# Kernel optimization log

Hardware: AMD Instinct MI355X
Metric: run time of the kernel (lower is better)

Reference implementation:

```python
import jax, jax.numpy as jnp
import numpy as np

N_NODES = 10000
N_EDGES = 70000
H = 128
L = 15  # message_passing_num
NODE_IN = 11  # 2 frame dims + 9 one-hot node types
EDGE_IN = 3
LN_EPS = 1e-5


def _mlp(x, W1, b1, W2, b2):
    return jax.nn.relu(x @ W1 + b1) @ W2 + b2


def _mlp_ln(x, W1, b1, W2, b2, g, b):
    h = _mlp(x, W1, b1, W2, b2)
    mu = jnp.mean(h, axis=-1, keepdims=True)
    var = jnp.var(h, axis=-1, keepdims=True)
    return (h - mu) * jax.lax.rsqrt(var + LN_EPS) * g + b


def setup_inputs() -> dict:
    key = jax.random.key(0)
    ks = iter(jax.random.split(key, 40))
    rn = lambda shp, s: (jax.random.normal(next(ks), shp, jnp.float32) * s)
    inp = {
        "node_type": jax.random.randint(next(ks), (N_NODES,), 0, 9, jnp.int32),
        "edge_index": jax.random.randint(next(ks), (2, N_EDGES), 0, N_NODES, jnp.int32),
        "frames": jax.random.normal(next(ks), (N_NODES, 2), jnp.float32),
        "edge_feats": jax.random.normal(next(ks), (N_EDGES, EDGE_IN), jnp.float32),
        "node_norm_mean": jax.random.normal(next(ks), (NODE_IN,), jnp.float32) * 0.1,
        "node_norm_std": jax.random.uniform(next(ks), (NODE_IN,), jnp.float32) + 0.5,
        "out_norm_mean": jax.random.normal(next(ks), (2,), jnp.float32) * 0.1,
        "out_norm_std": jax.random.uniform(next(ks), (2,), jnp.float32) + 0.5,
        # encoder node MLP (11 -> 128 -> 128, LayerNorm)
        "enc_nW1": rn((NODE_IN, H), NODE_IN ** -0.5), "enc_nb1": jnp.zeros((H,)),
        "enc_nW2": rn((H, H), H ** -0.5), "enc_nb2": jnp.zeros((H,)),
        "enc_nlng": jnp.ones((H,)), "enc_nlnb": jnp.zeros((H,)),
        # encoder edge MLP (3 -> 128 -> 128, LayerNorm)
        "enc_eW1": rn((EDGE_IN, H), EDGE_IN ** -0.5), "enc_eb1": jnp.zeros((H,)),
        "enc_eW2": rn((H, H), H ** -0.5), "enc_eb2": jnp.zeros((H,)),
        "enc_elng": jnp.ones((H,)), "enc_elnb": jnp.zeros((H,)),
        # L GNN blocks, stacked. Edge MLP: 3H -> H -> H (+LN); Node MLP: 2H -> H -> H (+LN)
        "eb_W1": rn((L, 3 * H, H), (3 * H) ** -0.5), "eb_b1": jnp.zeros((L, H)),
        "eb_W2": rn((L, H, H), H ** -0.5), "eb_b2": jnp.zeros((L, H)),
        "eb_lng": jnp.ones((L, H)), "eb_lnb": jnp.zeros((L, H)),
        "nb_W1": rn((L, 2 * H, H), (2 * H) ** -0.5), "nb_b1": jnp.zeros((L, H)),
        "nb_W2": rn((L, H, H), H ** -0.5), "nb_b2": jnp.zeros((L, H)),
        "nb_lng": jnp.ones((L, H)), "nb_lnb": jnp.zeros((L, H)),
        # decoder MLP (128 -> 128 -> 2, no LayerNorm)
        "dec_W1": rn((H, H), H ** -0.5), "dec_b1": jnp.zeros((H,)),
        "dec_W2": rn((H, 2), H ** -0.5), "dec_b2": jnp.zeros((2,)),
    }
    return inp


def reference(node_type, edge_index, frames, edge_feats,
              node_norm_mean, node_norm_std, out_norm_mean, out_norm_std,
              enc_nW1, enc_nb1, enc_nW2, enc_nb2, enc_nlng, enc_nlnb,
              enc_eW1, enc_eb1, enc_eW2, enc_eb2, enc_elng, enc_elnb,
              eb_W1, eb_b1, eb_W2, eb_b2, eb_lng, eb_lnb,
              nb_W1, nb_b1, nb_W2, nb_b2, nb_lng, nb_lnb,
              dec_W1, dec_b1, dec_W2, dec_b2):
    n_nodes = frames.shape[0]
    senders, receivers = edge_index[0], edge_index[1]

    # update_node_attr: concat(frames, one_hot(type, 9)) then normalize (eval mode)
    one_hot = jax.nn.one_hot(node_type, 9, dtype=frames.dtype)
    node_feats = jnp.concatenate([frames, one_hot], axis=1)  # [N, 11]
    node_attr = (node_feats - node_norm_mean) / node_norm_std

    # Encoder
    x = _mlp_ln(node_attr, enc_nW1, enc_nb1, enc_nW2, enc_nb2, enc_nlng, enc_nlnb)   # [N, H]
    e = _mlp_ln(edge_feats, enc_eW1, enc_eb1, enc_eW2, enc_eb2, enc_elng, enc_elnb)  # [E, H]

    # Processor: L residual GNN blocks (EdgeBlock then NodeBlock)
    def block(carry, p):
        x, e = carry
        (eW1, eb1, eW2, eb2, eg, ebn, nW1, nb1, nW2, nb2, ng, nbn) = p
        e_in = jnp.concatenate([x[senders], x[receivers], e], axis=-1)  # [E, 3H]
        e_new = _mlp_ln(e_in, eW1, eb1, eW2, eb2, eg, ebn)              # [E, H]
        agg = jax.ops.segment_sum(e_new, receivers, num_segments=n_nodes)  # [N, H]
        x_new = _mlp_ln(jnp.concatenate([x, agg], axis=-1), nW1, nb1, nW2, nb2, ng, nbn)
        return (x + x_new, e + e_new), None

    (x, e), _ = jax.lax.scan(
        block, (x, e),
        (eb_W1, eb_b1, eb_W2, eb_b2, eb_lng, eb_lnb,
         nb_W1, nb_b1, nb_W2, nb_b2, nb_lng, nb_lnb))

    # Decoder (no LayerNorm) + inverse output normalization (eval path)
    decoded = _mlp(x, dec_W1, dec_b1, dec_W2, dec_b2)  # [N, 2]
    velocity_update = decoded * out_norm_std + out_norm_mean
    return frames + velocity_update
```

## Files before the change

kernel.cpp:

```cpp
#include <hip/hip_runtime.h>
#include <hip/hip_bf16.h>

#define N_NODES 10000
#define N_EDGES 70000
#define NPAD 10112
#define EPAD 70016
#define H 128
#define NLAYERS 15
constexpr float LN_EPS = 1e-5f;

typedef __attribute__((ext_vector_type(8))) short short8;
typedef __attribute__((ext_vector_type(4))) float f32x4;

__device__ __forceinline__ float bf2f(unsigned int ulo16) {
    return __uint_as_float(ulo16 << 16);
}
__device__ __forceinline__ unsigned short f2bf(float f) {
    unsigned int x = __float_as_uint(f);
    x += 0x7fffu + ((x >> 16) & 1u);
    return (unsigned short)(x >> 16);
}

__global__ void prep_node(const int* __restrict__ nt, const float* __restrict__ frames,
                          const float* __restrict__ nm, const float* __restrict__ ns,
                          unsigned short* __restrict__ a16b) {
    int i = blockIdx.x * blockDim.x + threadIdx.x;
    if (i >= NPAD * 32) return;
    int n = i >> 5, k = i & 31;
    float v = 0.f;
    if (n < N_NODES && k < 11) {
        float raw = (k < 2) ? frames[n * 2 + k] : ((nt[n] == (k - 2)) ? 1.f : 0.f);
        v = (raw - nm[k]) / ns[k];
    }
    a16b[i] = f2bf(v);
}

__global__ void prep_edge(const float* __restrict__ ef, unsigned short* __restrict__ a4b) {
    int i = blockIdx.x * blockDim.x + threadIdx.x;
    if (i >= EPAD * 32) return;
    int e = i >> 5, k = i & 31;
    float v = (e < N_EDGES && k < 3) ? ef[e * 3 + k] : 0.f;
    a4b[i] = f2bf(v);
}

__global__ void transpose_w(const float* __restrict__ w, unsigned short* __restrict__ wt,
                            int Kr, int Kp, int nmat) {
    int i = blockIdx.x * blockDim.x + threadIdx.x;
    int total = nmat * 128 * Kp;
    if (i >= total) return;
    int m = i / (128 * Kp);
    int r = i % (128 * Kp);
    int c = r / Kp;
    int k = r % Kp;
    float v = (k < Kr) ? w[((size_t)m * Kr + k) * H + c] : 0.f;
    wt[i] = f2bf(v);
}

__global__ void hist_kernel(const int* __restrict__ rcv, int* __restrict__ counts) {
    int j = blockIdx.x * blockDim.x + threadIdx.x;
    if (j < N_EDGES) atomicAdd(&counts[rcv[j]], 1);
}

__global__ void scan_kernel(const int* __restrict__ counts, int* __restrict__ starts) {
    __shared__ int part[1024];
    const int CH = 10;
    int t = threadIdx.x;
    int base = t * CH;
    int loc[CH];
    int s = 0;
#pragma unroll
    for (int i = 0; i < CH; i++) {
        int idx = base + i;
        int c = (idx < N_NODES) ? counts[idx] : 0;
        loc[i] = s;
        s += c;
    }
    part[t] = s;
    __syncthreads();
    for (int off = 1; off < 1024; off <<= 1) {
        int v = (t >= off) ? part[t - off] : 0;
        __syncthreads();
        part[t] += v;
        __syncthreads();
    }
    int pre = (t > 0) ? part[t - 1] : 0;
#pragma unroll
    for (int i = 0; i < CH; i++) {
        int idx = base + i;
        if (idx < N_NODES) starts[idx] = pre + loc[i];
    }
}

__global__ void scatter_kernel(const int* __restrict__ rcv, const int* __restrict__ starts,
                               int* __restrict__ cursor, int* __restrict__ esorted) {
    int j = blockIdx.x * blockDim.x + threadIdx.x;
    if (j >= N_EDGES) return;
    int r = rcv[j];
    int p = starts[r] + atomicAdd(&cursor[r], 1);
    esorted[p] = j;
}

__global__ void agg_kernel(const unsigned short* __restrict__ enew,
                           const int* __restrict__ esorted,
                           const int* __restrict__ starts,
                           const int* __restrict__ counts,
                           unsigned short* __restrict__ aggb) {
    int n = blockIdx.x * 8 + (threadIdx.x >> 5);
    int l = threadIdx.x & 31;
    if (n >= N_NODES) return;
    float a0 = 0.f, a1 = 0.f, a2 = 0.f, a3 = 0.f;
    int s0 = starts[n], cnt = counts[n];
    for (int j = 0; j < cnt; ++j) {
        int e = esorted[s0 + j];
        uint2 v = *reinterpret_cast<const uint2*>(enew + (size_t)e * H + l * 4);
        a0 += bf2f(v.x & 0xffffu);
        a1 += bf2f(v.x >> 16);
        a2 += bf2f(v.y & 0xffffu);
        a3 += bf2f(v.y >> 16);
    }
    uint2 o;
    o.x = (unsigned int)f2bf(a0) | ((unsigned int)f2bf(a1) << 16);
    o.y = (unsigned int)f2bf(a2) | ((unsigned int)f2bf(a3) << 16);
    *reinterpret_cast<uint2*>(aggb + (size_t)n * H + l * 4) = o;
}

template <int K, int AMODE, int EPI, int WR>
__launch_bounds__(256)
__global__ void gemm_mfma(const unsigned short* __restrict__ A,
                          const unsigned short* __restrict__ Xb,
                          const unsigned short* __restrict__ Eb,
                          const unsigned short* __restrict__ Gb,
                          const int* __restrict__ snd,
                          const int* __restrict__ rcv,
                          const unsigned short* __restrict__ Bt,
                          const float* __restrict__ bias,
                          const float* __restrict__ lng,
                          const float* __restrict__ lnb,
                          unsigned short* __restrict__ out_bf,
                          float* __restrict__ out_fp,
                          unsigned short* __restrict__ enew_bf,
                          int nrows) {
    constexpr int BK = (K >= 64) ? 64 : K;
    constexpr int SA = BK + 8;
    constexpr int BM = 64 * WR;
    constexpr int KSTEP = BK / 32;
    __shared__ __attribute__((aligned(16))) unsigned short As[BM * SA];
    __shared__ __attribute__((aligned(16))) unsigned short Bs[H * SA];

    const int tid = threadIdx.x;
    const int wave = tid >> 6;
    const int lane = tid & 63;
    const int l15 = lane & 15;
    const int lhi = lane >> 4;
    const int row0 = blockIdx.x * BM;
    const int wrow = wave * 16 * WR;

    f32x4 acc[WR][8];
#pragma unroll
    for (int i = 0; i < WR; i++)
#pragma unroll
        for (int j = 0; j < 8; j++) acc[i][j] = (f32x4){0.f, 0.f, 0.f, 0.f};

    for (int kc = 0; kc < K; kc += BK) {
        constexpr int KQ = BK / 8;
        constexpr int LPT_A = BM * BK / 8 / 256;
#pragma unroll
        for (int it = 0; it < LPT_A; ++it) {
            int q = tid + it * 256;
            int r = q / KQ;
            int kq = q % KQ;
            int gk = kc + kq * 8;
            int grow = row0 + r;
            const unsigned short* src;
            if (AMODE == 0) {
                src = A + (size_t)grow * K + gk;
            } else if (AMODE == 1) {
                int e = (grow < nrows) ? grow : 0;
                if (gk < H)          src = Xb + (size_t)snd[e] * H + gk;
                else if (gk < 2 * H) src = Xb + (size_t)rcv[e] * H + (gk - H);
                else                 src = Eb + (size_t)grow * H + (gk - 2 * H);
            } else {
                if (gk < H) src = Xb + (size_t)grow * H + gk;
                else        src = Gb + (size_t)grow * H + (gk - H);
            }
            uint4 v = *reinterpret_cast<const uint4*>(src);
            *reinterpret_cast<uint4*>(&As[r * SA + kq * 8]) = v;
        }
        constexpr int LPT_B = H * BK / 8 / 256;
#pragma unroll
        for (int it = 0; it < LPT_B; ++it) {
            int q = tid + it * 256;
            int c = q / KQ;
            int kq = q % KQ;
            uint4 v = *reinterpret_cast<const uint4*>(Bt + (size_t)c * K + kc + kq * 8);
            *reinterpret_cast<uint4*>(&Bs[c * SA + kq * 8]) = v;
        }
        __syncthreads();
#pragma unroll
        for (int ks = 0; ks < KSTEP; ++ks) {
            short8 af[WR];
#pragma unroll
            for (int i = 0; i < WR; ++i)
                af[i] = *reinterpret_cast<const short8*>(
                    &As[(wrow + i * 16 + l15) * SA + ks * 32 + lhi * 8]);
#pragma unroll
            for (int j = 0; j < 8; ++j) {
                short8 bfr = *reinterpret_cast<const short8*>(
                    &Bs[(j * 16 + l15) * SA + ks * 32 + lhi * 8]);
#pragma unroll
                for (int i = 0; i < WR; ++i)
                    acc[i][j] = __builtin_amdgcn_mfma_f32_16x16x32_bf16(af[i], bfr, acc[i][j], 0, 0, 0);
            }
        }
        __syncthreads();
    }

    float bv[8], gv[8], lv[8];
#pragma unroll
    for (int j = 0; j < 8; ++j) {
        bv[j] = bias[j * 16 + l15];
        if (EPI >= 1) { gv[j] = lng[j * 16 + l15]; lv[j] = lnb[j * 16 + l15]; }
    }

#pragma unroll
    for (int i = 0; i < WR; ++i) {
#pragma unroll
        for (int r = 0; r < 4; ++r) {
            int row = row0 + wrow + i * 16 + lhi * 4 + r;
            if (EPI == 0) {
                if (row < nrows) {
#pragma unroll
                    for (int j = 0; j < 8; ++j) {
                        float v = acc[i][j][r] + bv[j];
                        v = v > 0.f ? v : 0.f;
                        out_bf[(size_t)row * H + j * 16 + l15] = f2bf(v);
                    }
                }
            } else {
                float v[8];
                float s = 0.f, s2 = 0.f;
#pragma unroll
                for (int j = 0; j < 8; ++j) {
                    v[j] = acc[i][j][r] + bv[j];
                    s += v[j];
                    s2 += v[j] * v[j];
                }
#pragma unroll
                for (int m = 1; m < 16; m <<= 1) {
                    s += __shfl_xor(s, m);
                    s2 += __shfl_xor(s2, m);
                }
                float mean = s * (1.f / 128.f);
                float var = s2 * (1.f / 128.f) - mean * mean;
                float rstd = rsqrtf(var + LN_EPS);
                if (row < nrows) {
#pragma unroll
                    for (int j = 0; j < 8; ++j) {
                        float o = (v[j] - mean) * rstd * gv[j] + lv[j];
                        size_t off = (size_t)row * H + j * 16 + l15;
                        if (EPI == 1) {
                            out_fp[off] = o;
                            out_bf[off] = f2bf(o);
                        } else if (EPI == 2) {
                            float nx = out_fp[off] + o;
                            out_fp[off] = nx;
                            out_bf[off] = f2bf(nx);
                        } else {
                            float ne = out_fp[off] + o;
                            out_fp[off] = ne;
                            out_bf[off] = f2bf(ne);
                            enew_bf[off] = f2bf(o);
                        }
                    }
                }
            }
        }
    }
}

__global__ void decoder_kernel(const float* __restrict__ x,
                               const float* __restrict__ frames,
                               const float* __restrict__ W1, const float* __restrict__ b1,
                               const float* __restrict__ W2, const float* __restrict__ b2,
                               const float* __restrict__ omean, const float* __restrict__ ostd,
                               float* __restrict__ outp) {
    __shared__ float xr[H];
    __shared__ float hr[H];
    __shared__ float red[2][2];
    int n = blockIdx.x;
    int t = threadIdx.x;
    xr[t] = x[n * H + t];
    __syncthreads();
    float acc = 0.f;
#pragma unroll 8
    for (int k = 0; k < H; k++) acc += xr[k] * W1[k * H + t];
    hr[t] = fmaxf(acc + b1[t], 0.f);
    __syncthreads();
    float p0 = hr[t] * W2[t * 2 + 0];
    float p1 = hr[t] * W2[t * 2 + 1];
#pragma unroll
    for (int m = 1; m < 64; m <<= 1) {
        p0 += __shfl_xor(p0, m);
        p1 += __shfl_xor(p1, m);
    }
    if ((t & 63) == 0) { red[t >> 6][0] = p0; red[t >> 6][1] = p1; }
    __syncthreads();
    if (t < 2) {
        float d = red[0][t] + red[1][t] + b2[t];
        outp[n * 2 + t] = frames[n * 2 + t] + d * ostd[t] + omean[t];
    }
}

extern "C" void kernel_launch(void* const* d_in, const int* in_sizes, int n_in,
                              void* d_out, int out_size, void* d_ws, size_t ws_size,
                              hipStream_t stream) {
    (void)in_sizes; (void)n_in; (void)out_size; (void)ws_size;
    const int*   node_type  = (const int*)  d_in[0];
    const int*   edge_index = (const int*)  d_in[1];
    const float* frames     = (const float*)d_in[2];
    const float* edge_feats = (const float*)d_in[3];
    const float* nmean      = (const float*)d_in[4];
    const float* nstd       = (const float*)d_in[5];
    const float* omean      = (const float*)d_in[6];
    const float* ostd       = (const float*)d_in[7];
    const float* enc_nW1    = (const float*)d_in[8];
    const float* enc_nb1    = (const float*)d_in[9];
    const float* enc_nW2    = (const float*)d_in[10];
    const float* enc_nb2    = (const float*)d_in[11];
    const float* enc_nlng   = (const float*)d_in[12];
    const float* enc_nlnb   = (const float*)d_in[13];
    const float* enc_eW1    = (const float*)d_in[14];
    const float* enc_eb1    = (const float*)d_in[15];
    const float* enc_eW2    = (const float*)d_in[16];
    const float* enc_eb2    = (const float*)d_in[17];
    const float* enc_elng   = (const float*)d_in[18];
    const float* enc_elnb   = (const float*)d_in[19];
    const float* eb_W1      = (const float*)d_in[20];
    const float* eb_b1      = (const float*)d_in[21];
    const float* eb_W2      = (const float*)d_in[22];
    const float* eb_b2      = (const float*)d_in[23];
    const float* eb_g       = (const float*)d_in[24];
    const float* eb_bn      = (const float*)d_in[25];
    const float* nb_W1      = (const float*)d_in[26];
    const float* nb_b1      = (const float*)d_in[27];
    const float* nb_W2      = (const float*)d_in[28];
    const float* nb_b2      = (const float*)d_in[29];
    const float* nb_g       = (const float*)d_in[30];
    const float* nb_bn      = (const float*)d_in[31];
    const float* dec_W1     = (const float*)d_in[32];
    const float* dec_b1     = (const float*)d_in[33];
    const float* dec_W2     = (const float*)d_in[34];
    const float* dec_b2     = (const float*)d_in[35];

    const int* snd = edge_index;
    const int* rcv = edge_index + N_EDGES;

    char* p = (char*)d_ws;
    auto alloc = [&](size_t bytes) {
        void* r = (void*)p;
        p += (bytes + 255) & ~(size_t)255;
        return r;
    };
    float* x_fp  = (float*)alloc((size_t)NPAD * H * 4);
    float* e_fp  = (float*)alloc((size_t)EPAD * H * 4);
    unsigned short* x_bf   = (unsigned short*)alloc((size_t)NPAD * H * 2);
    unsigned short* e_bf   = (unsigned short*)alloc((size_t)EPAD * H * 2);
    unsigned short* enew   = (unsigned short*)alloc((size_t)EPAD * H * 2);
    unsigned short* h_bf   = (unsigned short*)alloc((size_t)EPAD * H * 2);
    unsigned short* agg_bf = (unsigned short*)alloc((size_t)NPAD * H * 2);
    unsigned short* a16b   = (unsigned short*)alloc((size_t)NPAD * 32 * 2);
    unsigned short* a4b    = (unsigned short*)alloc((size_t)EPAD * 32 * 2);
    unsigned short* wt_en1 = (unsigned short*)alloc((size_t)128 * 32 * 2);
    unsigned short* wt_ee1 = (unsigned short*)alloc((size_t)128 * 32 * 2);
    unsigned short* wt_en2 = (unsigned short*)alloc((size_t)128 * 128 * 2);
    unsigned short* wt_ee2 = (unsigned short*)alloc((size_t)128 * 128 * 2);
    unsigned short* wt_eb1 = (unsigned short*)alloc((size_t)NLAYERS * 128 * 384 * 2);
    unsigned short* wt_eb2 = (unsigned short*)alloc((size_t)NLAYERS * 128 * 128 * 2);
    unsigned short* wt_nb1 = (unsigned short*)alloc((size_t)NLAYERS * 128 * 256 * 2);
    unsigned short* wt_nb2 = (unsigned short*)alloc((size_t)NLAYERS * 128 * 128 * 2);
    int* counts  = (int*)alloc((size_t)N_NODES * 4);
    int* starts  = (int*)alloc((size_t)N_NODES * 4);
    int* cursor  = (int*)alloc((size_t)N_NODES * 4);
    int* esorted = (int*)alloc((size_t)N_EDGES * 4);

    prep_node<<<(NPAD * 32 + 255) / 256, 256, 0, stream>>>(node_type, frames, nmean, nstd, a16b);
    prep_edge<<<(EPAD * 32 + 255) / 256, 256, 0, stream>>>(edge_feats, a4b);
    auto tw = [&](const float* w, unsigned short* wt, int Kr, int Kp, int nmat) {
        int total = nmat * 128 * Kp;
        transpose_w<<<(total + 255) / 256, 256, 0, stream>>>(w, wt, Kr, Kp, nmat);
    };
    tw(enc_nW1, wt_en1, 11, 32, 1);
    tw(enc_eW1, wt_ee1, 3, 32, 1);
    tw(enc_nW2, wt_en2, 128, 128, 1);
    tw(enc_eW2, wt_ee2, 128, 128, 1);
    tw(eb_W1, wt_eb1, 384, 384, NLAYERS);
    tw(eb_W2, wt_eb2, 128, 128, NLAYERS);
    tw(nb_W1, wt_nb1, 256, 256, NLAYERS);
    tw(nb_W2, wt_nb2, 128, 128, NLAYERS);

    hipMemsetAsync(counts, 0, (size_t)N_NODES * 4, stream);
    hipMemsetAsync(cursor, 0, (size_t)N_NODES * 4, stream);
    hist_kernel<<<(N_EDGES + 255) / 256, 256, 0, stream>>>(rcv, counts);
    scan_kernel<<<1, 1024, 0, stream>>>(counts, starts);
    scatter_kernel<<<(N_EDGES + 255) / 256, 256, 0, stream>>>(rcv, starts, cursor, esorted);

    const int gE = EPAD / 128;
    const int gN = NPAD / 64;
    const unsigned short* nu_ = nullptr;
    const int* ni_ = nullptr;
    const float* nf_ = nullptr;
    unsigned short* nm_ = nullptr;
    float* nfm_ = nullptr;

    gemm_mfma<32, 0, 0, 1><<<gN, 256, 0, stream>>>(a16b, nu_, nu_, nu_, ni_, ni_,
        wt_en1, enc_nb1, nf_, nf_, h_bf, nfm_, nm_, N_NODES);
    gemm_mfma<128, 0, 1, 1><<<gN, 256, 0, stream>>>(h_bf, nu_, nu_, nu_, ni_, ni_,
        wt_en2, enc_nb2, enc_nlng, enc_nlnb, x_bf, x_fp, nm_, N_NODES);
    gemm_mfma<32, 0, 0, 2><<<gE, 256, 0, stream>>>(a4b, nu_, nu_, nu_, ni_, ni_,
        wt_ee1, enc_eb1, nf_, nf_, h_bf, nfm_, nm_, N_EDGES);
    gemm_mfma<128, 0, 1, 2><<<gE, 256, 0, stream>>>(h_bf, nu_, nu_, nu_, ni_, ni_,
        wt_ee2, enc_eb2, enc_elng, enc_elnb, e_bf, e_fp, nm_, N_EDGES);

    for (int l = 0; l < NLAYERS; ++l) {
        gemm_mfma<384, 1, 0, 2><<<gE, 256, 0, stream>>>(nu_, x_bf, e_bf, nu_, snd, rcv,
            wt_eb1 + (size_t)l * 128 * 384, eb_b1 + l * H, nf_, nf_,
            h_bf, nfm_, nm_, N_EDGES);
        gemm_mfma<128, 0, 3, 2><<<gE, 256, 0, stream>>>(h_bf, nu_, nu_, nu_, ni_, ni_,
            wt_eb2 + (size_t)l * 128 * 128, eb_b2 + l * H, eb_g + l * H, eb_bn + l * H,
            e_bf, e_fp, enew, N_EDGES);
        agg_kernel<<<(N_NODES + 7) / 8, 256, 0, stream>>>(enew, esorted, starts, counts, agg_bf);
        gemm_mfma<256, 2, 0, 1><<<gN, 256, 0, stream>>>(nu_, x_bf, nu_, agg_bf, ni_, ni_,
            wt_nb1 + (size_t)l * 128 * 256, nb_b1 + l * H, nf_, nf_,
            h_bf, nfm_, nm_, N_NODES);
        gemm_mfma<128, 0, 2, 1><<<gN, 256, 0, stream>>>(h_bf, nu_, nu_, nu_, ni_, ni_,
            wt_nb2 + (size_t)l * 128 * 128, nb_b2 + l * H, nb_g + l * H, nb_bn + l * H,
            x_bf, x_fp, nm_, N_NODES);
    }

    decoder_kernel<<<N_NODES, 128, 0, stream>>>(x_fp, frames, dec_W1, dec_b1, dec_W2, dec_b2,
                                                omean, ostd, (float*)d_out);
}
```

Before: 1.460 ms.

## Fuse both MLP GEMMs into one kernel keeping hidden activations in LDS

Merges the two GEMMs of each MLP (first layer with ReLU, second layer with LayerNorm epilogue) into one kernel. The ReLU'd hidden tile is kept in shared memory and used directly as the A operand of the second GEMM, so the hidden h_bf buffer no longer round-trips through global memory and the launch count per layer halves. It also replaces the naive weight transpose with a shared-memory tiled transpose. The cost is more LDS per block (a hidden tile of up to 128x136 bf16 added), which may lower occupancy.

```diff
diff --git a/kernel.cpp b/kernel.cpp
--- a/kernel.cpp
+++ b/kernel.cpp
@@ -43,17 +43,29 @@
     a4b[i] = f2bf(v);
 }
 
-__global__ void transpose_w(const float* __restrict__ w, unsigned short* __restrict__ wt,
-                            int Kr, int Kp, int nmat) {
-    int i = blockIdx.x * blockDim.x + threadIdx.x;
-    int total = nmat * 128 * Kp;
-    if (i >= total) return;
-    int m = i / (128 * Kp);
-    int r = i % (128 * Kp);
-    int c = r / Kp;
-    int k = r % Kp;
-    float v = (k < Kr) ? w[((size_t)m * Kr + k) * H + c] : 0.f;
-    wt[i] = f2bf(v);
+__global__ void transpose_w_tiled(const float* __restrict__ w, unsigned short* __restrict__ wt,
+                                  int Kr, int Kp, int nmat) {
+    __shared__ float T[32][33];
+    int nkt = Kp / 32;
+    int bid = blockIdx.x;
+    int m = bid / (nkt * 4);
+    int rest = bid % (nkt * 4);
+    int kt = rest / 4, ct = rest % 4;
+    int t = threadIdx.x;
+    int tc = t & 31, tr = t >> 5;
+#pragma unroll
+    for (int rr = 0; rr < 4; ++rr) {
+        int k = kt * 32 + tr + rr * 8;
+        int c = ct * 32 + tc;
+        T[tr + rr * 8][tc] = (k < Kr) ? w[((size_t)m * Kr + k) * H + c] : 0.f;
+    }
+    __syncthreads();
+#pragma unroll
+    for (int rr = 0; rr < 4; ++rr) {
+        int c = ct * 32 + tr + rr * 8;
+        int k = kt * 32 + tc;
+        wt[((size_t)m * H + c) * Kp + k] = f2bf(T[tc][tr + rr * 8]);
+    }
 }
 
 __global__ void hist_kernel(const int* __restrict__ rcv, int* __restrict__ counts) {
@@ -124,28 +136,32 @@
     *reinterpret_cast<uint2*>(aggb + (size_t)n * H + l * 4) = o;
 }
 
-template <int K, int AMODE, int EPI, int WR>
+template <int K1, int AMODE, int EPI, int WR>
 __launch_bounds__(256)
-__global__ void gemm_mfma(const unsigned short* __restrict__ A,
+__global__ void mlp_fused(const unsigned short* __restrict__ A,
                           const unsigned short* __restrict__ Xb,
                           const unsigned short* __restrict__ Eb,
                           const unsigned short* __restrict__ Gb,
                           const int* __restrict__ snd,
                           const int* __restrict__ rcv,
-                          const unsigned short* __restrict__ Bt,
-                          const float* __restrict__ bias,
+                          const unsigned short* __restrict__ Bt1,
+                          const float* __restrict__ bias1,
+                          const unsigned short* __restrict__ Bt2,
+                          const float* __restrict__ bias2,
                           const float* __restrict__ lng,
                           const float* __restrict__ lnb,
                           unsigned short* __restrict__ out_bf,
                           float* __restrict__ out_fp,
                           unsigned short* __restrict__ enew_bf,
                           int nrows) {
-    constexpr int BK = (K >= 64) ? 64 : K;
-    constexpr int SA = BK + 8;
+    constexpr int BK1 = (K1 >= 64) ? 64 : K1;
+    constexpr int SA = BK1 + 8;
+    constexpr int SB = 72;
+    constexpr int SH = H + 8;
     constexpr int BM = 64 * WR;
-    constexpr int KSTEP = BK / 32;
     __shared__ __attribute__((aligned(16))) unsigned short As[BM * SA];
-    __shared__ __attribute__((aligned(16))) unsigned short Bs[H * SA];
+    __shared__ __attribute__((aligned(16))) unsigned short Bs[H * SB];
+    __shared__ __attribute__((aligned(16))) unsigned short Hs[BM * SH];
 
     const int tid = threadIdx.x;
     const int wave = tid >> 6;
@@ -161,9 +177,9 @@
 #pragma unroll
         for (int j = 0; j < 8; j++) acc[i][j] = (f32x4){0.f, 0.f, 0.f, 0.f};
 
-    for (int kc = 0; kc < K; kc += BK) {
-        constexpr int KQ = BK / 8;
-        constexpr int LPT_A = BM * BK / 8 / 256;
+    for (int kc = 0; kc < K1; kc += BK1) {
+        constexpr int KQ = BK1 / 8;
+        constexpr int LPT_A = BM * KQ / 256;
 #pragma unroll
         for (int it = 0; it < LPT_A; ++it) {
             int q = tid + it * 256;
@@ -173,7 +189,7 @@
             int grow = row0 + r;
             const unsigned short* src;
             if (AMODE == 0) {
-                src = A + (size_t)grow * K + gk;
+                src = A + (size_t)grow * K1 + gk;
             } else if (AMODE == 1) {
                 int e = (grow < nrows) ? grow : 0;
                 if (gk < H)          src = Xb + (size_t)snd[e] * H + gk;
@@ -186,18 +202,18 @@
             uint4 v = *reinterpret_cast<const uint4*>(src);
             *reinterpret_cast<uint4*>(&As[r * SA + kq * 8]) = v;
         }
-        constexpr int LPT_B = H * BK / 8 / 256;
+        constexpr int LPT_B = H * KQ / 256;
 #pragma unroll
         for (int it = 0; it < LPT_B; ++it) {
             int q = tid + it * 256;
             int c = q / KQ;
             int kq = q % KQ;
-            uint4 v = *reinterpret_cast<const uint4*>(Bt + (size_t)c * K + kc + kq * 8);
-            *reinterpret_cast<uint4*>(&Bs[c * SA + kq * 8]) = v;
-        }
-        __syncthreads();
-#pragma unroll
-        for (int ks = 0; ks < KSTEP; ++ks) {
+            uint4 v = *reinterpret_cast<const uint4*>(Bt1 + (size_t)c * K1 + kc + kq * 8);
+            *reinterpret_cast<uint4*>(&Bs[c * SB + kq * 8]) = v;
+        }
+        __syncthreads();
+#pragma unroll
+        for (int ks = 0; ks < BK1 / 32; ++ks) {
             short8 af[WR];
 #pragma unroll
             for (int i = 0; i < WR; ++i)
@@ -206,7 +222,7 @@
 #pragma unroll
             for (int j = 0; j < 8; ++j) {
                 short8 bfr = *reinterpret_cast<const short8*>(
-                    &Bs[(j * 16 + l15) * SA + ks * 32 + lhi * 8]);
+                    &Bs[(j * 16 + l15) * SB + ks * 32 + lhi * 8]);
 #pragma unroll
                 for (int i = 0; i < WR; ++i)
                     acc[i][j] = __builtin_amdgcn_mfma_f32_16x16x32_bf16(af[i], bfr, acc[i][j], 0, 0, 0);
@@ -215,11 +231,63 @@
         __syncthreads();
     }
 
+    {
+        float b1v[8];
+#pragma unroll
+        for (int j = 0; j < 8; ++j) b1v[j] = bias1[j * 16 + l15];
+#pragma unroll
+        for (int i = 0; i < WR; ++i)
+#pragma unroll
+            for (int r = 0; r < 4; ++r) {
+                int rl = wrow + i * 16 + lhi * 4 + r;
+#pragma unroll
+                for (int j = 0; j < 8; ++j) {
+                    float v = acc[i][j][r] + b1v[j];
+                    Hs[rl * SH + j * 16 + l15] = f2bf(v > 0.f ? v : 0.f);
+                }
+            }
+    }
+
+#pragma unroll
+    for (int i = 0; i < WR; i++)
+#pragma unroll
+        for (int j = 0; j < 8; j++) acc[i][j] = (f32x4){0.f, 0.f, 0.f, 0.f};
+
+    for (int kc = 0; kc < H; kc += 64) {
+        __syncthreads();
+#pragma unroll
+        for (int it = 0; it < 4; ++it) {
+            int q = tid + it * 256;
+            int c = q >> 3;
+            int kq = q & 7;
+            uint4 v = *reinterpret_cast<const uint4*>(Bt2 + (size_t)c * H + kc + kq * 8);
+            *reinterpret_cast<uint4*>(&Bs[c * SB + kq * 8]) = v;
+        }
+        __syncthreads();
+#pragma unroll
+        for (int ks = 0; ks < 2; ++ks) {
+            short8 af[WR];
+#pragma unroll
+            for (int i = 0; i < WR; ++i)
+                af[i] = *reinterpret_cast<const short8*>(
+                    &Hs[(wrow + i * 16 + l15) * SH + kc + ks * 32 + lhi * 8]);
+#pragma unroll
+            for (int j = 0; j < 8; ++j) {
+                short8 bfr = *reinterpret_cast<const short8*>(
+                    &Bs[(j * 16 + l15) * SB + ks * 32 + lhi * 8]);
+#pragma unroll
+                for (int i = 0; i < WR; ++i)
+                    acc[i][j] = __builtin_amdgcn_mfma_f32_16x16x32_bf16(af[i], bfr, acc[i][j], 0, 0, 0);
+            }
+        }
+    }
+
     float bv[8], gv[8], lv[8];
 #pragma unroll
     for (int j = 0; j < 8; ++j) {
-        bv[j] = bias[j * 16 + l15];
-        if (EPI >= 1) { gv[j] = lng[j * 16 + l15]; lv[j] = lnb[j * 16 + l15]; }
+        bv[j] = bias2[j * 16 + l15];
+        gv[j] = lng[j * 16 + l15];
+        lv[j] = lnb[j * 16 + l15];
     }
 
 #pragma unroll
@@ -227,50 +295,39 @@
 #pragma unroll
         for (int r = 0; r < 4; ++r) {
             int row = row0 + wrow + i * 16 + lhi * 4 + r;
-            if (EPI == 0) {
-                if (row < nrows) {
-#pragma unroll
-                    for (int j = 0; j < 8; ++j) {
-                        float v = acc[i][j][r] + bv[j];
-                        v = v > 0.f ? v : 0.f;
-                        out_bf[(size_t)row * H + j * 16 + l15] = f2bf(v);
-                    }
-                }
-            } else {
-                float v[8];
-                float s = 0.f, s2 = 0.f;
+            float v[8];
+            float s = 0.f, s2 = 0.f;
+#pragma unroll
+            for (int j = 0; j < 8; ++j) {
+                v[j] = acc[i][j][r] + bv[j];
+                s += v[j];
+                s2 += v[j] * v[j];
+            }
+#pragma unroll
+            for (int m = 1; m < 16; m <<= 1) {
+                s += __shfl_xor(s, m);
+                s2 += __shfl_xor(s2, m);
+            }
+            float mean = s * (1.f / 128.f);
+            float var = s2 * (1.f / 128.f) - mean * mean;
+            float rstd = rsqrtf(var + LN_EPS);
+            if (row < nrows) {
 #pragma unroll
                 for (int j = 0; j < 8; ++j) {
-                    v[j] = acc[i][j][r] + bv[j];
-                    s += v[j];
-                    s2 += v[j] * v[j];
-                }
-#pragma unroll
-                for (int m = 1; m < 16; m <<= 1) {
-                    s += __shfl_xor(s, m);
-                    s2 += __shfl_xor(s2, m);
-                }
-                float mean = s * (1.f / 128.f);
-                float var = s2 * (1.f / 128.f) - mean * mean;
-                float rstd = rsqrtf(var + LN_EPS);
-                if (row < nrows) {
-#pragma unroll
-                    for (int j = 0; j < 8; ++j) {
-                        float o = (v[j] - mean) * rstd * gv[j] + lv[j];
-                        size_t off = (size_t)row * H + j * 16 + l15;
-                        if (EPI == 1) {
-                            out_fp[off] = o;
-                            out_bf[off] = f2bf(o);
-                        } else if (EPI == 2) {
-                            float nx = out_fp[off] + o;
-                            out_fp[off] = nx;
-                            out_bf[off] = f2bf(nx);
-                        } else {
-                            float ne = out_fp[off] + o;
-                            out_fp[off] = ne;
-                            out_bf[off] = f2bf(ne);
-                            enew_bf[off] = f2bf(o);
-                        }
+                    float o = (v[j] - mean) * rstd * gv[j] + lv[j];
+                    size_t off = (size_t)row * H + j * 16 + l15;
+                    if (EPI == 1) {
+                        out_fp[off] = o;
+                        out_bf[off] = f2bf(o);
+                    } else if (EPI == 2) {
+                        float nx = out_fp[off] + o;
+                        out_fp[off] = nx;
+                        out_bf[off] = f2bf(nx);
+                    } else {
+                        float ne = out_fp[off] + o;
+                        out_fp[off] = ne;
+                        out_bf[off] = f2bf(ne);
+                        enew_bf[off] = f2bf(o);
                     }
                 }
             }
@@ -366,7 +423,6 @@
     unsigned short* x_bf   = (unsigned short*)alloc((size_t)NPAD * H * 2);
     unsigned short* e_bf   = (unsigned short*)alloc((size_t)EPAD * H * 2);
     unsigned short* enew   = (unsigned short*)alloc((size_t)EPAD * H * 2);
-    unsigned short* h_bf   = (unsigned short*)alloc((size_t)EPAD * H * 2);
     unsigned short* agg_bf = (unsigned short*)alloc((size_t)NPAD * H * 2);
     unsigned short* a16b   = (unsigned short*)alloc((size_t)NPAD * 32 * 2);
     unsigned short* a4b    = (unsigned short*)alloc((size_t)EPAD * 32 * 2);
@@ -386,8 +442,8 @@
     prep_node<<<(NPAD * 32 + 255) / 256, 256, 0, stream>>>(node_type, frames, nmean, nstd, a16b);
     prep_edge<<<(EPAD * 32 + 255) / 256, 256, 0, stream>>>(edge_feats, a4b);
     auto tw = [&](const float* w, unsigned short* wt, int Kr, int Kp, int nmat) {
-        int total = nmat * 128 * Kp;
-        transpose_w<<<(total + 255) / 256, 256, 0, stream>>>(w, wt, Kr, Kp, nmat);
+        int blocks = nmat * (Kp / 32) * 4;
+        transpose_w_tiled<<<blocks, 256, 0, stream>>>(w, wt, Kr, Kp, nmat);
     };
     tw(enc_nW1, wt_en1, 11, 32, 1);
     tw(enc_eW1, wt_ee1, 3, 32, 1);
@@ -408,31 +464,23 @@
     const int gN = NPAD / 64;
     const unsigned short* nu_ = nullptr;
     const int* ni_ = nullptr;
-    const float* nf_ = nullptr;
     unsigned short* nm_ = nullptr;
-    float* nfm_ = nullptr;
-
-    gemm_mfma<32, 0, 0, 1><<<gN, 256, 0, stream>>>(a16b, nu_, nu_, nu_, ni_, ni_,
-        wt_en1, enc_nb1, nf_, nf_, h_bf, nfm_, nm_, N_NODES);
-    gemm_mfma<128, 0, 1, 1><<<gN, 256, 0, stream>>>(h_bf, nu_, nu_, nu_, ni_, ni_,
-        wt_en2, enc_nb2, enc_nlng, enc_nlnb, x_bf, x_fp, nm_, N_NODES);
-    gemm_mfma<32, 0, 0, 2><<<gE, 256, 0, stream>>>(a4b, nu_, nu_, nu_, ni_, ni_,
-        wt_ee1, enc_eb1, nf_, nf_, h_bf, nfm_, nm_, N_EDGES);
-    gemm_mfma<128, 0, 1, 2><<<gE, 256, 0, stream>>>(h_bf, nu_, nu_, nu_, ni_, ni_,
-        wt_ee2, enc_eb2, enc_elng, enc_elnb, e_bf, e_fp, nm_, N_EDGES);
+
+    mlp_fused<32, 0, 1, 1><<<gN, 256, 0, stream>>>(a16b, nu_, nu_, nu_, ni_, ni_,
+        wt_en1, enc_nb1, wt_en2, enc_nb2, enc_nlng, enc_nlnb,
+        x_bf, x_fp, nm_, N_NODES);
+    mlp_fused<32, 0, 1, 2><<<gE, 256, 0, stream>>>(a4b, nu_, nu_, nu_, ni_, ni_,
+        wt_ee1, enc_eb1, wt_ee2, enc_eb2, enc_elng, enc_elnb,
+        e_bf, e_fp, nm_, N_EDGES);
 
     for (int l = 0; l < NLAYERS; ++l) {
-        gemm_mfma<384, 1, 0, 2><<<gE, 256, 0, stream>>>(nu_, x_bf, e_bf, nu_, snd, rcv,
-            wt_eb1 + (size_t)l * 128 * 384, eb_b1 + l * H, nf_, nf_,
-            h_bf, nfm_, nm_, N_EDGES);
-        gemm_mfma<128, 0, 3, 2><<<gE, 256, 0, stream>>>(h_bf, nu_, nu_, nu_, ni_, ni_,
+        mlp_fused<384, 1, 3, 2><<<gE, 256, 0, stream>>>(nu_, x_bf, e_bf, nu_, snd, rcv,
+            wt_eb1 + (size_t)l * 128 * 384, eb_b1 + l * H,
             wt_eb2 + (size_t)l * 128 * 128, eb_b2 + l * H, eb_g + l * H, eb_bn + l * H,
             e_bf, e_fp, enew, N_EDGES);
         agg_kernel<<<(N_NODES + 7) / 8, 256, 0, stream>>>(enew, esorted, starts, counts, agg_bf);
-        gemm_mfma<256, 2, 0, 1><<<gN, 256, 0, stream>>>(nu_, x_bf, nu_, agg_bf, ni_, ni_,
-            wt_nb1 + (size_t)l * 128 * 256, nb_b1 + l * H, nf_, nf_,
-            h_bf, nfm_, nm_, N_NODES);
-        gemm_mfma<128, 0, 2, 1><<<gN, 256, 0, stream>>>(h_bf, nu_, nu_, nu_, ni_, ni_,
+        mlp_fused<256, 2, 2, 1><<<gN, 256, 0, stream>>>(nu_, x_bf, nu_, agg_bf, ni_, ni_,
+            wt_nb1 + (size_t)l * 128 * 256, nb_b1 + l * H,
             wt_nb2 + (size_t)l * 128 * 128, nb_b2 + l * H, nb_g + l * H, nb_bn + l * H,
             x_bf, x_fp, nm_, N_NODES);
     }
```

After: 1.181 ms. -19.2%, faster.
